# Kernel optimization log

Hardware: AMD Instinct MI355X
Metric: run time of the kernel (lower is better)

The kernel has to match this reference:

```python
import jax, jax.numpy as jnp
import numpy as np

EEG_DIM, CLIP_DIM, NUM_SUBJECTS, BATCH = 256, 512, 13, 16384
EPS = 1e-12  # torch F.normalize eps


def setup_inputs() -> dict:
    key = jax.random.key(0)
    k0, k1, k2, k3, k4, k5 = jax.random.split(key, 6)
    # Kaiming-uniform-ish init for per-subject Linear layers
    lim1 = 1.0 / np.sqrt(EEG_DIM)
    lim2 = 1.0 / np.sqrt(CLIP_DIM)
    return {
        "eeg_emb": jax.random.normal(k0, (BATCH, EEG_DIM), dtype=jnp.float32),
        "subject_ids": jax.random.randint(k1, (BATCH,), 0, NUM_SUBJECTS),
        "W1": jax.random.uniform(k2, (NUM_SUBJECTS, EEG_DIM, CLIP_DIM), jnp.float32, -lim1, lim1),
        "b1": jax.random.uniform(k3, (NUM_SUBJECTS, CLIP_DIM), jnp.float32, -lim1, lim1),
        "W2": jax.random.uniform(k4, (NUM_SUBJECTS, CLIP_DIM, CLIP_DIM), jnp.float32, -lim2, lim2),
        "b2": jax.random.uniform(k5, (NUM_SUBJECTS, CLIP_DIM), jnp.float32, -lim2, lim2),
    }


def reference(eeg_emb, subject_ids, W1, b1, W2, b2):
    # Hard-routed per-subject 2-layer MLP. We compute all subject heads densely
    # (b s h) and select the row for each sample's subject id -- vectorized
    # equivalent of the original per-subject gather/scatter loop.
    h = jax.nn.relu(jnp.einsum('bd,sdh->bsh', eeg_emb, W1) + b1)  # [B,S,H]
    y = jnp.einsum('bsh,sho->bso', h, W2) + b2                     # [B,S,O]
    out = jnp.take_along_axis(y, subject_ids[:, None, None], axis=1)[:, 0, :]  # [B,O]
    # F.normalize(p=2, dim=1): x / max(||x||, eps)
    norm = jnp.linalg.norm(out, axis=1, keepdims=True)
    return out / jnp.maximum(norm, EPS)
```

## Files before the change

### kernel.cpp

```cpp
#include <hip/hip_runtime.h>
#include <hip/hip_bf16.h>


#define BATCH 16384
#define EEG 256
#define CLIP 512
#define NSUB 13

#define M_BCNT 0
#define M_SOFF 832
#define M_TOT  846
#define M_C128 859
#define M_IDX  896

typedef unsigned short u16;
typedef __attribute__((ext_vector_type(8))) short short8;
typedef __attribute__((ext_vector_type(4))) float f32x4;

__device__ __forceinline__ u16 f2bf(float f) {
    union { float f; unsigned int u; } v; v.f = f;
    unsigned int u = v.u;
    unsigned int r = (u + 0x7FFFu + ((u >> 16) & 1u)) >> 16;
    return (u16)r;
}

__global__ __launch_bounds__(256) void convert_pack(
    const float* __restrict__ W1, const float* __restrict__ W2,
    u16* __restrict__ w1p, u16* __restrict__ w2p,
    const int* __restrict__ sid, int* __restrict__ meta) {
    __shared__ u16 T[64][72];
    __shared__ int hh[NSUB];
    int b = blockIdx.x;
    const float* src; u16* dstbase; int ksteps;
    int s, kt, g;
    if (b < 416) {
        s = b >> 5; int t = b & 31;
        kt = t >> 3; g = t & 7;
        ksteps = 8;
        src = W1 + (size_t)s * EEG * CLIP;
        dstbase = w1p + (size_t)s * CLIP * EEG;
    } else {
        b -= 416; s = b >> 6; int t = b & 63;
        kt = t >> 3; g = t & 7;
        ksteps = 16;
        src = W2 + (size_t)s * CLIP * CLIP;
        dstbase = w2p + (size_t)s * CLIP * CLIP;
    }
    int k0 = kt << 6, n0 = g << 6;
    int tid = threadIdx.x;
    int rk = tid >> 2;
    int cg = (tid & 3) << 4;
    const float4* p4 = reinterpret_cast<const float4*>(src + (size_t)(k0 + rk) * CLIP + n0 + cg);
    #pragma unroll
    for (int jj = 0; jj < 4; ++jj) {
        float4 v = p4[jj];
        T[cg + jj * 4 + 0][rk] = f2bf(v.x);
        T[cg + jj * 4 + 1][rk] = f2bf(v.y);
        T[cg + jj * 4 + 2][rk] = f2bf(v.z);
        T[cg + jj * 4 + 3][rk] = f2bf(v.w);
    }
    __syncthreads();
    int colin = tid & 63, sl = (tid >> 6) & 3;
    #pragma unroll
    for (int half = 0; half < 2; ++half) {
        int t = kt * 2 + half;
        u16* dst = dstbase + ((size_t)(g * ksteps + t)) * 2048 + sl * 512 + colin * 8;
        *reinterpret_cast<short8*>(dst) =
            *reinterpret_cast<const short8*>(&T[colin][half * 32 + sl * 8]);
    }
    if (blockIdx.x < 64) {
        if (tid < NSUB) hh[tid] = 0;
        __syncthreads();
        atomicAdd(&hh[sid[blockIdx.x * 256 + tid]], 1);
        __syncthreads();
        if (tid < NSUB) meta[M_BCNT + blockIdx.x * NSUB + tid] = hh[tid];
    }
}

__global__ __launch_bounds__(256) void scanscatter_k(
    const int* __restrict__ sid, int* __restrict__ meta) {
    __shared__ int cnt[64][NSUB];
    __shared__ int so[NSUB + 1], myoff[NSUB], tot[NSUB];
    __shared__ int h[NSUB];
    int tid = threadIdx.x;
    for (int i = tid; i < 64 * NSUB; i += 256)
        cnt[i / NSUB][i % NSUB] = meta[M_BCNT + i];
    if (tid < NSUB) h[tid] = 0;
    __syncthreads();
    if (tid < NSUB) {
        int run = 0, mine = 0;
        for (int b = 0; b < 64; ++b) {
            if (b == (int)blockIdx.x) mine = run;
            run += cnt[b][tid];
        }
        tot[tid] = run; myoff[tid] = mine;
    }
    __syncthreads();
    if (tid == 0) {
        int off = 0;
        for (int s = 0; s < NSUB; ++s) { so[s] = off; off += tot[s]; }
        so[NSUB] = off;
    }
    __syncthreads();
    if (blockIdx.x == 0) {
        if (tid < NSUB + 1) meta[M_SOFF + tid] = so[tid];
        if (tid < NSUB) meta[M_TOT + tid] = tot[tid];
        if (tid == 0) {
            int c128 = 0;
            for (int s = 0; s < NSUB; ++s) {
                meta[M_C128 + s] = c128;
                c128 += (tot[s] + 127) >> 7;
            }
            meta[M_C128 + NSUB] = c128;
        }
    }
    int i = blockIdx.x * 256 + tid;
    int s = sid[i];
    int r = atomicAdd(&h[s], 1);
    meta[M_IDX + so[s] + myoff[s] + r] = i;
}

__global__ __launch_bounds__(1024) void mlp_k(
    const float* __restrict__ X, const float* __restrict__ b1,
    const float* __restrict__ b2, const u16* __restrict__ w1p,
    const u16* __restrict__ w2p, const int* __restrict__ meta,
    float* __restrict__ out) {

    __shared__ u16 Hs[128 * 520];
    __shared__ float partial[128 * 8];
    __shared__ float scalev[128];
    __shared__ int info[4];
    __shared__ int rowidx[128];
    __shared__ int cobuf[14], sobuf[14], totbuf[NSUB];

    int tid = threadIdx.x;

    int nwg = gridDim.x;
    int q = nwg >> 3, r = nwg & 7;
    int xcd = blockIdx.x & 7, idx = blockIdx.x >> 3;
    int bid = (xcd < r) ? xcd * (q + 1) + idx : r * (q + 1) + (xcd - r) * q + idx;

    if (tid < 14) { cobuf[tid] = meta[M_C128 + tid]; sobuf[tid] = meta[M_SOFF + tid]; }
    if (tid < NSUB) totbuf[tid] = meta[M_TOT + tid];
    __syncthreads();
    if (tid == 0) {
        int total = cobuf[NSUB];
        if (bid < total) {
            int s = 0;
            while (s < NSUB && !(bid >= cobuf[s] && bid < cobuf[s + 1])) s++;
            int chunk = bid - cobuf[s];
            info[0] = s;
            info[1] = sobuf[s] + chunk * 128;
            info[2] = min(128, totbuf[s] - chunk * 128);
        } else info[0] = -1;
    }
    __syncthreads();
    if (info[0] < 0) return;
    int s = info[0], rowbase = info[1], nrows = info[2];
    if (tid < 128) rowidx[tid] = meta[M_IDX + rowbase + min(tid, nrows - 1)];

    int wave = tid >> 6, lane = tid & 63;
    int c = lane & 15, gl = lane >> 4;
    int wm = wave >> 3, wn = wave & 7;
    int col0 = wn * 64;
    const u16* w1c = w1p + (size_t)s * CLIP * EEG + (size_t)wn * 8 * 2048;
    const u16* w2c = w2p + (size_t)s * CLIP * CLIP + (size_t)wn * 16 * 2048;

    u16* Xc = Hs;

    f32x4 acc[4][4];
    #pragma unroll
    for (int mi = 0; mi < 4; ++mi)
        #pragma unroll
        for (int ni = 0; ni < 4; ++ni)
            acc[mi][ni] = (f32x4){0.f, 0.f, 0.f, 0.f};

    int srow = tid >> 3, sl8 = tid & 7;

    for (int kc = 0; kc < 4; ++kc) {
        __syncthreads();
        {
            const float4* xp = reinterpret_cast<const float4*>(
                X + (size_t)rowidx[srow] * EEG) + kc * 16;
            u16* xd = &Xc[srow * 72];
            #pragma unroll
            for (int half = 0; half < 2; ++half) {
                int j = sl8 + half * 8;
                float4 v = xp[j];
                union { u16 u[4]; uint2 qq; } pk;
                pk.u[0] = f2bf(v.x); pk.u[1] = f2bf(v.y);
                pk.u[2] = f2bf(v.z); pk.u[3] = f2bf(v.w);
                *reinterpret_cast<uint2*>(&xd[j * 4]) = pk.qq;
            }
        }
        __syncthreads();
        #pragma unroll
        for (int k0 = 0; k0 < 64; k0 += 32) {
            int t = kc * 2 + (k0 >> 5);
            short8 a[4], bb[4];
            #pragma unroll
            for (int ni = 0; ni < 4; ++ni)
                bb[ni] = *reinterpret_cast<const short8*>(
                    &w1c[(size_t)t * 2048 + gl * 512 + (ni * 16 + c) * 8]);
            #pragma unroll
            for (int mi = 0; mi < 4; ++mi)
                a[mi] = *reinterpret_cast<const short8*>(
                    &Xc[(wm * 64 + mi * 16 + c) * 72 + k0 + gl * 8]);
            #pragma unroll
            for (int mi = 0; mi < 4; ++mi)
                #pragma unroll
                for (int ni = 0; ni < 4; ++ni)
                    acc[mi][ni] = __builtin_amdgcn_mfma_f32_16x16x32_bf16(a[mi], bb[ni], acc[mi][ni], 0, 0, 0);
        }
    }
    __syncthreads();

    {
        float bias1[4];
        #pragma unroll
        for (int ni = 0; ni < 4; ++ni) bias1[ni] = b1[s * CLIP + col0 + ni * 16 + c];
        #pragma unroll
        for (int mi = 0; mi < 4; ++mi)
            #pragma unroll
            for (int ni = 0; ni < 4; ++ni)
                #pragma unroll
                for (int i = 0; i < 4; ++i) {
                    float h = fmaxf(acc[mi][ni][i] + bias1[ni], 0.f);
                    Hs[(wm * 64 + mi * 16 + gl * 4 + i) * 520 + col0 + ni * 16 + c] = f2bf(h);
                }
    }
    __syncthreads();

    #pragma unroll
    for (int mi = 0; mi < 4; ++mi)
        #pragma unroll
        for (int ni = 0; ni < 4; ++ni)
            acc[mi][ni] = (f32x4){0.f, 0.f, 0.f, 0.f};

    #pragma unroll 4
    for (int k0 = 0; k0 < CLIP; k0 += 32) {
        int t = k0 >> 5;
        short8 a[4], bb[4];
        #pragma unroll
        for (int ni = 0; ni < 4; ++ni)
            bb[ni] = *reinterpret_cast<const short8*>(
                &w2c[(size_t)t * 2048 + gl * 512 + (ni * 16 + c) * 8]);
        #pragma unroll
        for (int mi = 0; mi < 4; ++mi)
            a[mi] = *reinterpret_cast<const short8*>(
                &Hs[(wm * 64 + mi * 16 + c) * 520 + k0 + gl * 8]);
        #pragma unroll
        for (int mi = 0; mi < 4; ++mi)
            #pragma unroll
            for (int ni = 0; ni < 4; ++ni)
                acc[mi][ni] = __builtin_amdgcn_mfma_f32_16x16x32_bf16(a[mi], bb[ni], acc[mi][ni], 0, 0, 0);
    }

    float sq[4][4];
    {
        float bias2[4];
        #pragma unroll
        for (int ni = 0; ni < 4; ++ni) bias2[ni] = b2[s * CLIP + col0 + ni * 16 + c];
        #pragma unroll
        for (int mi = 0; mi < 4; ++mi)
            #pragma unroll
            for (int i = 0; i < 4; ++i) sq[mi][i] = 0.f;
        #pragma unroll
        for (int mi = 0; mi < 4; ++mi)
            #pragma unroll
            for (int ni = 0; ni < 4; ++ni)
                #pragma unroll
                for (int i = 0; i < 4; ++i) {
                    float v = acc[mi][ni][i] + bias2[ni];
                    acc[mi][ni][i] = v;
                    sq[mi][i] += v * v;
                }
    }
    #pragma unroll
    for (int m = 1; m < 16; m <<= 1)
        #pragma unroll
        for (int mi = 0; mi < 4; ++mi)
            #pragma unroll
            for (int i = 0; i < 4; ++i)
                sq[mi][i] += __shfl_xor(sq[mi][i], m);

    if (c == 0) {
        #pragma unroll
        for (int mi = 0; mi < 4; ++mi)
            #pragma unroll
            for (int i = 0; i < 4; ++i)
                partial[(wm * 64 + mi * 16 + gl * 4 + i) * 8 + wn] = sq[mi][i];
    }
    __syncthreads();
    if (tid < 128) {
        float t = 0.f;
        #pragma unroll
        for (int w = 0; w < 8; ++w) t += partial[tid * 8 + w];
        scalev[tid] = 1.f / fmaxf(sqrtf(t), 1e-12f);
    }
    __syncthreads();

    #pragma unroll
    for (int mi = 0; mi < 4; ++mi)
        #pragma unroll
        for (int i = 0; i < 4; ++i) {
            int row = wm * 64 + mi * 16 + gl * 4 + i;
            if (row < nrows) {
                float sc = scalev[row];
                float* op = out + (size_t)rowidx[row] * CLIP + col0 + c;
                #pragma unroll
                for (int ni = 0; ni < 4; ++ni)
                    __builtin_nontemporal_store(acc[mi][ni][i] * sc, op + ni * 16);
            }
        }
}

extern "C" void kernel_launch(void* const* d_in, const int* in_sizes, int n_in,
                              void* d_out, int out_size, void* d_ws, size_t ws_size,
                              hipStream_t stream) {
    const float* eeg = (const float*)d_in[0];
    const int* sid   = (const int*)d_in[1];
    const float* W1  = (const float*)d_in[2];
    const float* b1  = (const float*)d_in[3];
    const float* W2  = (const float*)d_in[4];
    const float* b2  = (const float*)d_in[5];
    float* out = (float*)d_out;

    u16* w1p = (u16*)d_ws;
    u16* w2p = w1p + (size_t)NSUB * CLIP * EEG;
    int* meta = (int*)(w2p + (size_t)NSUB * CLIP * CLIP);

    convert_pack<<<1248, 256, 0, stream>>>(W1, W2, w1p, w2p, sid, meta);
    scanscatter_k<<<64, 256, 0, stream>>>(sid, meta);
    mlp_k<<<BATCH / 128 + NSUB, 1024, 0, stream>>>(eeg, b1, b2, w1p, w2p, meta, out);
}
```

Measured before the change: 49.94 us.

## Shrink row tile to 112 with 8 waves, stage weights through LDS via async loads

Changes each block from 16 waves covering 128 rows to 8 waves each covering all 112 rows by 64 columns, so every wave reuses its weight fragment across 7 M-tiles instead of 4. Weight tiles are now streamed into LDS with global_load_lds, and the W2 loop prefetches the next tile while computing the current one. The tile-count metadata and grid size change to match the 112-row chunks. The larger accumulator array raises register pressure, and the vmcnt waits and sched barriers may serialise loads against MFMA work.

New measurement: 51.30 us (median of 2 runs). 1.03x slower.

```diff
diff --git a/kernel.cpp b/kernel.cpp
--- a/kernel.cpp
+++ b/kernel.cpp
@@ -10,7 +10,7 @@
 #define M_BCNT 0
 #define M_SOFF 832
 #define M_TOT  846
-#define M_C128 859
+#define M_C112 859
 #define M_IDX  896
 
 typedef unsigned short u16;
@@ -106,12 +106,12 @@
         if (tid < NSUB + 1) meta[M_SOFF + tid] = so[tid];
         if (tid < NSUB) meta[M_TOT + tid] = tot[tid];
         if (tid == 0) {
-            int c128 = 0;
+            int c112 = 0;
             for (int s = 0; s < NSUB; ++s) {
-                meta[M_C128 + s] = c128;
-                c128 += (tot[s] + 127) >> 7;
+                meta[M_C112 + s] = c112;
+                c112 += (tot[s] + 111) / 112;
             }
-            meta[M_C128 + NSUB] = c128;
+            meta[M_C112 + NSUB] = c112;
         }
     }
     int i = blockIdx.x * 256 + tid;
@@ -120,17 +120,18 @@
     meta[M_IDX + so[s] + myoff[s] + r] = i;
 }
 
-__global__ __launch_bounds__(1024) void mlp_k(
+__global__ __launch_bounds__(512) void mlp_k(
     const float* __restrict__ X, const float* __restrict__ b1,
     const float* __restrict__ b2, const u16* __restrict__ w1p,
     const u16* __restrict__ w2p, const int* __restrict__ meta,
     float* __restrict__ out) {
 
-    __shared__ u16 Hs[128 * 520];
-    __shared__ float partial[128 * 8];
-    __shared__ float scalev[128];
+    __shared__ u16 Hs[112 * 520];
+    __shared__ u16 Wl[8 * 2048];
+    __shared__ float partial[112 * 8];
+    __shared__ float scalev[112];
     __shared__ int info[4];
-    __shared__ int rowidx[128];
+    __shared__ int rowidx[112];
     __shared__ int cobuf[14], sobuf[14], totbuf[NSUB];
 
     int tid = threadIdx.x;
@@ -140,7 +141,7 @@
     int xcd = blockIdx.x & 7, idx = blockIdx.x >> 3;
     int bid = (xcd < r) ? xcd * (q + 1) + idx : r * (q + 1) + (xcd - r) * q + idx;
 
-    if (tid < 14) { cobuf[tid] = meta[M_C128 + tid]; sobuf[tid] = meta[M_SOFF + tid]; }
+    if (tid < 14) { cobuf[tid] = meta[M_C112 + tid]; sobuf[tid] = meta[M_SOFF + tid]; }
     if (tid < NSUB) totbuf[tid] = meta[M_TOT + tid];
     __syncthreads();
     if (tid == 0) {
@@ -150,42 +151,51 @@
             while (s < NSUB && !(bid >= cobuf[s] && bid < cobuf[s + 1])) s++;
             int chunk = bid - cobuf[s];
             info[0] = s;
-            info[1] = sobuf[s] + chunk * 128;
-            info[2] = min(128, totbuf[s] - chunk * 128);
+            info[1] = sobuf[s] + chunk * 112;
+            info[2] = min(112, totbuf[s] - chunk * 112);
         } else info[0] = -1;
     }
     __syncthreads();
     if (info[0] < 0) return;
     int s = info[0], rowbase = info[1], nrows = info[2];
-    if (tid < 128) rowidx[tid] = meta[M_IDX + rowbase + min(tid, nrows - 1)];
+    if (tid < 112) rowidx[tid] = meta[M_IDX + rowbase + min(tid, nrows - 1)];
 
     int wave = tid >> 6, lane = tid & 63;
     int c = lane & 15, gl = lane >> 4;
-    int wm = wave >> 3, wn = wave & 7;
-    int col0 = wn * 64;
-    const u16* w1c = w1p + (size_t)s * CLIP * EEG + (size_t)wn * 8 * 2048;
-    const u16* w2c = w2p + (size_t)s * CLIP * CLIP + (size_t)wn * 16 * 2048;
+    int col0 = wave * 64;
+    const u16* w1c = w1p + (size_t)s * CLIP * EEG + (size_t)wave * 8 * 2048;
+    const u16* w2c = w2p + (size_t)s * CLIP * CLIP + (size_t)wave * 16 * 2048;
+    u16* wl = &Wl[wave * 2048];
+
+#define STAGE_LDS(srcp) do {                                                     \
+        _Pragma("unroll")                                                        \
+        for (int _it = 0; _it < 4; ++_it)                                        \
+            __builtin_amdgcn_global_load_lds(                                    \
+                (const __attribute__((address_space(1))) unsigned int*)          \
+                    ((srcp) + _it * 512 + lane * 8),                             \
+                (__attribute__((address_space(3))) unsigned int*)(wl + _it * 512), \
+                16, 0, 0);                                                       \
+    } while (0)
 
     u16* Xc = Hs;
 
-    f32x4 acc[4][4];
-    #pragma unroll
-    for (int mi = 0; mi < 4; ++mi)
+    f32x4 acc[7][4];
+    #pragma unroll
+    for (int mi = 0; mi < 7; ++mi)
         #pragma unroll
         for (int ni = 0; ni < 4; ++ni)
             acc[mi][ni] = (f32x4){0.f, 0.f, 0.f, 0.f};
 
-    int srow = tid >> 3, sl8 = tid & 7;
+    int srow = min(tid >> 2, 111), sq4 = tid & 3;
 
     for (int kc = 0; kc < 4; ++kc) {
         __syncthreads();
         {
             const float4* xp = reinterpret_cast<const float4*>(
-                X + (size_t)rowidx[srow] * EEG) + kc * 16;
-            u16* xd = &Xc[srow * 72];
-            #pragma unroll
-            for (int half = 0; half < 2; ++half) {
-                int j = sl8 + half * 8;
+                X + (size_t)rowidx[srow] * EEG) + kc * 16 + sq4 * 4;
+            u16* xd = &Xc[srow * 72 + sq4 * 16];
+            #pragma unroll
+            for (int j = 0; j < 4; ++j) {
                 float4 v = xp[j];
                 union { u16 u[4]; uint2 qq; } pk;
                 pk.u[0] = f2bf(v.x); pk.u[1] = f2bf(v.y);
@@ -195,19 +205,21 @@
         }
         __syncthreads();
         #pragma unroll
-        for (int k0 = 0; k0 < 64; k0 += 32) {
-            int t = kc * 2 + (k0 >> 5);
-            short8 a[4], bb[4];
+        for (int half = 0; half < 2; ++half) {
+            int t = kc * 2 + half;
+            STAGE_LDS(w1c + (size_t)t * 2048);
+            asm volatile("s_waitcnt vmcnt(0)" ::: "memory");
+            __builtin_amdgcn_sched_barrier(0);
+            short8 bb[4], a[7];
             #pragma unroll
             for (int ni = 0; ni < 4; ++ni)
-                bb[ni] = *reinterpret_cast<const short8*>(
-                    &w1c[(size_t)t * 2048 + gl * 512 + (ni * 16 + c) * 8]);
-            #pragma unroll
-            for (int mi = 0; mi < 4; ++mi)
+                bb[ni] = *reinterpret_cast<const short8*>(&wl[gl * 512 + (ni * 16 + c) * 8]);
+            #pragma unroll
+            for (int mi = 0; mi < 7; ++mi)
                 a[mi] = *reinterpret_cast<const short8*>(
-                    &Xc[(wm * 64 + mi * 16 + c) * 72 + k0 + gl * 8]);
-            #pragma unroll
-            for (int mi = 0; mi < 4; ++mi)
+                    &Xc[(mi * 16 + c) * 72 + half * 32 + gl * 8]);
+            #pragma unroll
+            for (int mi = 0; mi < 7; ++mi)
                 #pragma unroll
                 for (int ni = 0; ni < 4; ++ni)
                     acc[mi][ni] = __builtin_amdgcn_mfma_f32_16x16x32_bf16(a[mi], bb[ni], acc[mi][ni], 0, 0, 0);
@@ -220,53 +232,58 @@
         #pragma unroll
         for (int ni = 0; ni < 4; ++ni) bias1[ni] = b1[s * CLIP + col0 + ni * 16 + c];
         #pragma unroll
-        for (int mi = 0; mi < 4; ++mi)
+        for (int mi = 0; mi < 7; ++mi)
             #pragma unroll
             for (int ni = 0; ni < 4; ++ni)
                 #pragma unroll
                 for (int i = 0; i < 4; ++i) {
                     float h = fmaxf(acc[mi][ni][i] + bias1[ni], 0.f);
-                    Hs[(wm * 64 + mi * 16 + gl * 4 + i) * 520 + col0 + ni * 16 + c] = f2bf(h);
+                    Hs[(mi * 16 + gl * 4 + i) * 520 + col0 + ni * 16 + c] = f2bf(h);
                 }
     }
     __syncthreads();
 
     #pragma unroll
-    for (int mi = 0; mi < 4; ++mi)
+    for (int mi = 0; mi < 7; ++mi)
         #pragma unroll
         for (int ni = 0; ni < 4; ++ni)
             acc[mi][ni] = (f32x4){0.f, 0.f, 0.f, 0.f};
 
-    #pragma unroll 4
-    for (int k0 = 0; k0 < CLIP; k0 += 32) {
-        int t = k0 >> 5;
-        short8 a[4], bb[4];
+    STAGE_LDS(w2c);
+    for (int t = 0; t < 16; ++t) {
+        asm volatile("s_waitcnt vmcnt(0)" ::: "memory");
+        __builtin_amdgcn_sched_barrier(0);
+        short8 bb[4];
         #pragma unroll
         for (int ni = 0; ni < 4; ++ni)
-            bb[ni] = *reinterpret_cast<const short8*>(
-                &w2c[(size_t)t * 2048 + gl * 512 + (ni * 16 + c) * 8]);
-        #pragma unroll
-        for (int mi = 0; mi < 4; ++mi)
+            bb[ni] = *reinterpret_cast<const short8*>(&wl[gl * 512 + (ni * 16 + c) * 8]);
+        asm volatile("s_waitcnt lgkmcnt(0)" ::: "memory");
+        __builtin_amdgcn_sched_barrier(0);
+        if (t < 15) STAGE_LDS(w2c + (size_t)(t + 1) * 2048);
+        short8 a[7];
+        #pragma unroll
+        for (int mi = 0; mi < 7; ++mi)
             a[mi] = *reinterpret_cast<const short8*>(
-                &Hs[(wm * 64 + mi * 16 + c) * 520 + k0 + gl * 8]);
-        #pragma unroll
-        for (int mi = 0; mi < 4; ++mi)
+                &Hs[(mi * 16 + c) * 520 + t * 32 + gl * 8]);
+        #pragma unroll
+        for (int mi = 0; mi < 7; ++mi)
             #pragma unroll
             for (int ni = 0; ni < 4; ++ni)
                 acc[mi][ni] = __builtin_amdgcn_mfma_f32_16x16x32_bf16(a[mi], bb[ni], acc[mi][ni], 0, 0, 0);
     }
-
-    float sq[4][4];
+#undef STAGE_LDS
+
+    float sq[7][4];
     {
         float bias2[4];
         #pragma unroll
         for (int ni = 0; ni < 4; ++ni) bias2[ni] = b2[s * CLIP + col0 + ni * 16 + c];
         #pragma unroll
-        for (int mi = 0; mi < 4; ++mi)
+        for (int mi = 0; mi < 7; ++mi)
             #pragma unroll
             for (int i = 0; i < 4; ++i) sq[mi][i] = 0.f;
         #pragma unroll
-        for (int mi = 0; mi < 4; ++mi)
+        for (int mi = 0; mi < 7; ++mi)
             #pragma unroll
             for (int ni = 0; ni < 4; ++ni)
                 #pragma unroll
@@ -279,20 +296,20 @@
     #pragma unroll
     for (int m = 1; m < 16; m <<= 1)
         #pragma unroll
-        for (int mi = 0; mi < 4; ++mi)
+        for (int mi = 0; mi < 7; ++mi)
             #pragma unroll
             for (int i = 0; i < 4; ++i)
                 sq[mi][i] += __shfl_xor(sq[mi][i], m);
 
     if (c == 0) {
         #pragma unroll
-        for (int mi = 0; mi < 4; ++mi)
+        for (int mi = 0; mi < 7; ++mi)
             #pragma unroll
             for (int i = 0; i < 4; ++i)
-                partial[(wm * 64 + mi * 16 + gl * 4 + i) * 8 + wn] = sq[mi][i];
-    }
-    __syncthreads();
-    if (tid < 128) {
+                partial[(mi * 16 + gl * 4 + i) * 8 + wave] = sq[mi][i];
+    }
+    __syncthreads();
+    if (tid < 112) {
         float t = 0.f;
         #pragma unroll
         for (int w = 0; w < 8; ++w) t += partial[tid * 8 + w];
@@ -301,10 +318,10 @@
     __syncthreads();
 
     #pragma unroll
-    for (int mi = 0; mi < 4; ++mi)
+    for (int mi = 0; mi < 7; ++mi)
         #pragma unroll
         for (int i = 0; i < 4; ++i) {
-            int row = wm * 64 + mi * 16 + gl * 4 + i;
+            int row = mi * 16 + gl * 4 + i;
             if (row < nrows) {
                 float sc = scalev[row];
                 float* op = out + (size_t)rowidx[row] * CLIP + col0 + c;
@@ -332,5 +349,5 @@
 
     convert_pack<<<1248, 256, 0, stream>>>(W1, W2, w1p, w2p, sid, meta);
     scanscatter_k<<<64, 256, 0, stream>>>(sid, meta);
-    mlp_k<<<BATCH / 128 + NSUB, 1024, 0, stream>>>(eeg, b1, b2, w1p, w2p, meta, out);
-}
+    mlp_k<<<BATCH / 112 + NSUB + 1, 512, 0, stream>>>(eeg, b1, b2, w1p, w2p, meta, out);
+}
```
